# Optimization experiments

Measured on AMD Instinct MI355X. Metric: run time of the kernel, lower is better.

Reference implementation:

```python
import jax, jax.numpy as jnp
import numpy as np

N = 100000
E = 1600000
D = 128      # input_dim == hidden_dim
C = 40       # output_dim
L = 3        # num_layers
EPS = 1e-12  # F.normalize eps


def setup_inputs() -> dict:
    key = jax.random.key(0)
    ks = jax.random.split(key, 8)
    x = jax.random.normal(ks[0], (N, D), dtype=jnp.float32)
    edge_index = jax.random.randint(ks[1], (2, E), 0, N, dtype=jnp.int64)
    s = 1.0 / np.sqrt(D)
    # SAGEConv: lin_l (neighbor path, with bias), lin_r (root path, no bias)
    Wl = jax.random.uniform(ks[2], (L, D, D), jnp.float32, -s, s)
    bl = jax.random.uniform(ks[3], (L, D), jnp.float32, -s, s)
    Wr = jax.random.uniform(ks[4], (L, D, D), jnp.float32, -s, s)
    Wlin = jax.random.uniform(ks[5], (C, D), jnp.float32, -s, s)
    blin = jax.random.uniform(ks[6], (C,), jnp.float32, -s, s)
    return {"x": x, "edge_index": edge_index, "Wl": Wl, "bl": bl,
            "Wr": Wr, "Wlin": Wlin, "blin": blin}


def reference(x, edge_index, Wl, bl, Wr, Wlin, blin):
    src, dst = edge_index[0], edge_index[1]
    # in-degree counts for mean aggregation (computed once, reused per layer)
    cnt = jax.ops.segment_sum(jnp.ones((E,), jnp.float32), dst, num_segments=N)
    inv_cnt = (1.0 / jnp.maximum(cnt, 1.0))[:, None]  # [N,1]
    z = x
    for i in range(L):
        msg = z[src]  # gather [E, D]
        agg = jax.ops.segment_sum(msg, dst, num_segments=N) * inv_cnt  # mean [N, D]
        out = agg @ Wl[i].T + bl[i] + z @ Wr[i].T
        # SAGEConv normalize=True: L2 normalize per node
        nrm = jnp.linalg.norm(out, axis=-1, keepdims=True)
        out = out / jnp.maximum(nrm, EPS)
        z = jax.nn.relu(out)  # dropout p=0 -> identity
    return z @ Wlin.T + blin  # [N, C]
```

## Files before the change

### kernel.cpp

```cpp
#include <hip/hip_runtime.h>


typedef __bf16 bf16x8 __attribute__((ext_vector_type(8)));
typedef float  f32x4  __attribute__((ext_vector_type(4)));

#define MFMA16(a, b, c) __builtin_amdgcn_mfma_f32_16x16x32_bf16((a), (b), (c), 0, 0, 0)

__device__ __forceinline__ unsigned rne_bf16(float f) {
  unsigned u = __float_as_uint(f);
  unsigned r = u + 0x7FFFu + ((u >> 16) & 1u);
  return r >> 16;
}

__device__ __forceinline__ float bf_lo(unsigned u) { return __uint_as_float(u << 16); }
__device__ __forceinline__ float bf_hi(unsigned u) { return __uint_as_float(u & 0xFFFF0000u); }


__global__ __launch_bounds__(256) void histA_k(const int* __restrict__ dst,
                                               int* __restrict__ ghist, int E) {
  __shared__ int h[128];
  const int tid = threadIdx.x;
  if (tid < 128) h[tid] = 0;
  __syncthreads();
  const int e0 = blockIdx.x * 2048;
#pragma unroll
  for (int j = 0; j < 8; ++j) {
    int e = e0 + j * 256 + tid;
    if (e < E) atomicAdd(&h[dst[e] >> 10], 1);
  }
  __syncthreads();
  if (tid < 128 && h[tid]) atomicAdd(&ghist[tid], h[tid]);
}

__global__ void cscan_k(const int* __restrict__ ghist, int* __restrict__ cbase,
                        int* __restrict__ gcur, int E) {
  __shared__ int sd[128];
  const int tid = threadIdx.x;
  int v = ghist[tid];
  sd[tid] = v;
  __syncthreads();
  for (int off = 1; off < 128; off <<= 1) {
    int u = (tid >= off) ? sd[tid - off] : 0;
    __syncthreads();
    sd[tid] += u;
    __syncthreads();
  }
  int excl = sd[tid] - v;
  cbase[tid] = excl;
  gcur[tid] = excl;
  if (tid == 127) cbase[128] = sd[127];
}

__global__ __launch_bounds__(256) void bucketA_k(
    const int* __restrict__ src, const int* __restrict__ dst,
    int* __restrict__ gcur, unsigned* __restrict__ coarse, int E, int nc) {
  __shared__ int hist[128];
  __shared__ int sd[128];
  __shared__ int lpos[128];
  __shared__ int gbase[128];
  __shared__ unsigned stage[2048];
  __shared__ unsigned char sbuck[2048];

  const int tid = threadIdx.x;
  const int e0 = blockIdx.x * 2048;

  if (tid < 128) hist[tid] = 0;
  __syncthreads();

  int bv[8], pk[8];
#pragma unroll
  for (int j = 0; j < 8; ++j) {
    int e = e0 + j * 256 + tid;
    bv[j] = -1;
    if (e < E) {
      int s = src[e], d = dst[e];
      bv[j] = d >> 10;
      pk[j] = s | ((d & 1023) << 17);
      atomicAdd(&hist[bv[j]], 1);
    }
  }
  __syncthreads();

  if (tid < 128) sd[tid] = hist[tid];
  __syncthreads();
  for (int off = 1; off < 128; off <<= 1) {
    int t = 0;
    if (tid < 128 && tid >= off) t = sd[tid - off];
    __syncthreads();
    if (tid < 128) sd[tid] += t;
    __syncthreads();
  }
  if (tid < 128) {
    int excl = sd[tid] - hist[tid];
    lpos[tid] = excl;
    gbase[tid] = (tid < nc && hist[tid] > 0) ? atomicAdd(&gcur[tid], hist[tid]) : 0;
  }
  __syncthreads();

#pragma unroll
  for (int j = 0; j < 8; ++j) {
    if (bv[j] >= 0) {
      int slot = atomicAdd(&lpos[bv[j]], 1);
      stage[slot] = (unsigned)pk[j];
      sbuck[slot] = (unsigned char)bv[j];
    }
  }
  __syncthreads();

  const int total = sd[127];
  for (int i = tid; i < total; i += 256) {
    int b = sbuck[i];
    int excl = sd[b] - hist[b];
    coarse[gbase[b] + (i - excl)] = stage[i];
  }
}

__global__ __launch_bounds__(256) void bucketB_k(
    const int* __restrict__ cbase, const unsigned* __restrict__ coarse,
    int* __restrict__ esrc, int* __restrict__ offsets,
    float* __restrict__ inv_cnt, int n, int E) {
  __shared__ int hcnt[1024];
  __shared__ int cur[1024];
  __shared__ int sd[256];

  const int tid = threadIdx.x;
  const int b = blockIdx.x;
  const int base = b * 1024;
  const int nn = (n - base < 1024) ? (n - base) : 1024;
  const int cbeg = cbase[b];
  const int cend = cbase[b + 1];

  for (int j = tid; j < 1024; j += 256) hcnt[j] = 0;
  __syncthreads();
  for (int idx = cbeg + tid; idx < cend; idx += 256)
    atomicAdd(&hcnt[coarse[idx] >> 17], 1);
  __syncthreads();

  int b0 = hcnt[tid * 4], b1 = hcnt[tid * 4 + 1];
  int b2 = hcnt[tid * 4 + 2], b3 = hcnt[tid * 4 + 3];
  int tot = b0 + b1 + b2 + b3;
  sd[tid] = tot;
  __syncthreads();
  for (int off = 1; off < 256; off <<= 1) {
    int u = (tid >= off) ? sd[tid - off] : 0;
    __syncthreads();
    sd[tid] += u;
    __syncthreads();
  }
  int excl = cbeg + sd[tid] - tot;
  cur[tid * 4]     = excl;
  cur[tid * 4 + 1] = excl + b0;
  cur[tid * 4 + 2] = excl + b0 + b1;
  cur[tid * 4 + 3] = excl + b0 + b1 + b2;
  __syncthreads();

  for (int j = tid; j < nn; j += 256) {
    offsets[base + j] = cur[j];
    int c = hcnt[j] > 1 ? hcnt[j] : 1;
    inv_cnt[base + j] = 1.0f / (float)c;
  }
  if (tid == 0 && base + nn >= n) offsets[n] = cend;
  __syncthreads();

  for (int idx = cbeg + tid; idx < cend; idx += 256) {
    unsigned p = coarse[idx];
    int pos = atomicAdd(&cur[p >> 17], 1);
    esrc[pos] = (int)(p & 0x1FFFFu);
  }
}

__global__ void to_bf16_k(const float4* __restrict__ in, uint2* __restrict__ out, int n4) {
  int i = blockIdx.x * 256 + threadIdx.x;
  if (i >= n4) return;
  float4 f = in[i];
  uint2 o;
  o.x = rne_bf16(f.x) | (rne_bf16(f.y) << 16);
  o.y = rne_bf16(f.z) | (rne_bf16(f.w) << 16);
  out[i] = o;
}

__global__ void wfrag_prep_k(const float* __restrict__ Wl, const float* __restrict__ Wr,
                             unsigned short* __restrict__ wfrag) {
  int id = blockIdx.x * 256 + threadIdx.x;
  if (id >= 3 * 2 * 8 * 8 * 64) return;
  int l = id & 63;
  int c = (id >> 6) & 7;
  int t = (id >> 9) & 7;
  int p = (id >> 12) & 1;
  int layer = id >> 13;
  int col = t * 16 + (l & 15);
  int kbase = c * 32 + (l >> 4) * 8;
  unsigned short* dst = wfrag + (size_t)layer * 65536 +
                        ((((size_t)p * 8 + t) * 8 + c) * 64 + l) * 8;
#pragma unroll
  for (int j = 0; j < 8; ++j) {
    int k = kbase + j;
    float w = (k < 128) ? Wl[layer * 16384 + col * 128 + k]
                        : Wr[layer * 16384 + col * 128 + (k - 128)];
    unsigned h = rne_bf16(w);
    unsigned o;
    if (p == 0) o = h;
    else o = rne_bf16(w - __uint_as_float(h << 16));
    dst[j] = (unsigned short)o;
  }
}

__global__ void wlin_frag_k(const float* __restrict__ Wlin, unsigned short* __restrict__ wlf) {
  int id = blockIdx.x * 256 + threadIdx.x;
  if (id >= 3 * 4 * 64) return;
  int l = id & 63;
  int c = (id >> 6) & 3;
  int t = id >> 8;
  int col = t * 16 + (l & 15);
  int kbase = c * 32 + (l >> 4) * 8;
  unsigned short* dst = wlf + (size_t)id * 8;
#pragma unroll
  for (int j = 0; j < 8; ++j) {
    float w = (col < 40) ? Wlin[col * 128 + kbase + j] : 0.f;
    dst[j] = (unsigned short)rne_bf16(w);
  }
}

__global__ void aggregate_k(const unsigned short* __restrict__ zb,
                            const int* __restrict__ offsets,
                            const int* __restrict__ esrc,
                            const float* __restrict__ inv_cnt,
                            float* __restrict__ agg, int n) {
  int w = (blockIdx.x * 256 + threadIdx.x) >> 6;
  int lane = threadIdx.x & 63;
  if (w >= n) return;
  int beg = offsets[w], end = offsets[w + 1];
  int cnt = end - beg;
  int q = lane >> 4;
  int l16 = lane & 15;
  float a0 = 0.f, a1 = 0.f, a2 = 0.f, a3 = 0.f;
  float a4 = 0.f, a5 = 0.f, a6 = 0.f, a7 = 0.f;
  int t = 0;
  for (; t + 16 <= cnt; t += 16) {
#pragma unroll
    for (int u = 0; u < 4; ++u) {
      int s = esrc[beg + t + 4 * u + q];
      uint4 d = *(const uint4*)(zb + (size_t)s * 128 + l16 * 8);
      a0 += bf_lo(d.x); a1 += bf_hi(d.x);
      a2 += bf_lo(d.y); a3 += bf_hi(d.y);
      a4 += bf_lo(d.z); a5 += bf_hi(d.z);
      a6 += bf_lo(d.w); a7 += bf_hi(d.w);
    }
  }
  for (; t + 4 <= cnt; t += 4) {
    int s = esrc[beg + t + q];
    uint4 d = *(const uint4*)(zb + (size_t)s * 128 + l16 * 8);
    a0 += bf_lo(d.x); a1 += bf_hi(d.x);
    a2 += bf_lo(d.y); a3 += bf_hi(d.y);
    a4 += bf_lo(d.z); a5 += bf_hi(d.z);
    a6 += bf_lo(d.w); a7 += bf_hi(d.w);
  }
  if (t < cnt) {
    int e = t + q;
    float m = (e < cnt) ? 1.f : 0.f;
    int ec = (e < cnt) ? (beg + e) : (end - 1);
    int s = esrc[ec];
    uint4 d = *(const uint4*)(zb + (size_t)s * 128 + l16 * 8);
    a0 = fmaf(m, bf_lo(d.x), a0); a1 = fmaf(m, bf_hi(d.x), a1);
    a2 = fmaf(m, bf_lo(d.y), a2); a3 = fmaf(m, bf_hi(d.y), a3);
    a4 = fmaf(m, bf_lo(d.z), a4); a5 = fmaf(m, bf_hi(d.z), a5);
    a6 = fmaf(m, bf_lo(d.w), a6); a7 = fmaf(m, bf_hi(d.w), a7);
  }
#pragma unroll
  for (int m = 16; m <= 32; m <<= 1) {
    a0 += __shfl_xor(a0, m); a1 += __shfl_xor(a1, m);
    a2 += __shfl_xor(a2, m); a3 += __shfl_xor(a3, m);
    a4 += __shfl_xor(a4, m); a5 += __shfl_xor(a5, m);
    a6 += __shfl_xor(a6, m); a7 += __shfl_xor(a7, m);
  }
  if (q == 0) {
    float ic = inv_cnt[w];
    float* op = agg + (size_t)w * 128 + l16 * 8;
    *(float4*)op = make_float4(a0 * ic, a1 * ic, a2 * ic, a3 * ic);
    *(float4*)(op + 4) = make_float4(a4 * ic, a5 * ic, a6 * ic, a7 * ic);
  }
}

__global__ __launch_bounds__(256, 2) void sage_layer_mfma_k(
    const unsigned short* __restrict__ zb, const float* __restrict__ agg,
    const unsigned short* __restrict__ wf, const float* __restrict__ bl,
    unsigned short* __restrict__ out_bf, int n, int ntiles) {
  __shared__ unsigned short Ah_s[32 * 256];
  __shared__ unsigned short Al_s[32 * 128];
  __shared__ float psum[2][4][16];

  const int lane = threadIdx.x & 63;
  const int wv = threadIdx.x >> 6;
  const int g = lane >> 4;
  const int rl = lane & 15;

  const bf16x8* wfv = (const bf16x8*)wf;
  const int t0 = wv * 2, t1 = wv * 2 + 1;
  bf16x8 Bh0[8], Bh1[8], Bl0[8], Bl1[8];
#pragma unroll
  for (int c = 0; c < 8; ++c) {
    Bh0[c] = wfv[((0 * 8 + t0) * 8 + c) * 64 + lane];
    Bh1[c] = wfv[((0 * 8 + t1) * 8 + c) * 64 + lane];
    Bl0[c] = wfv[((1 * 8 + t0) * 8 + c) * 64 + lane];
    Bl1[c] = wfv[((1 * 8 + t1) * 8 + c) * 64 + lane];
  }
  const float b0 = bl[t0 * 16 + rl];
  const float b1 = bl[t1 * 16 + rl];

  char* pAh = (char*)Ah_s;
  char* pAl = (char*)Al_s;

  for (int tile = blockIdx.x; tile < ntiles; tile += gridDim.x) {
    const int v0 = tile * 32;

#pragma unroll
    for (int q = 0; q < 4; ++q) {
      int lin = q * 1024 + threadIdx.x * 4;
      int r = lin >> 7;
      int col = lin & 127;
      int v = v0 + r; v = (v < n) ? v : (n - 1);
      float4 f = *(const float4*)(agg + (size_t)v * 128 + col);
      unsigned h0 = rne_bf16(f.x), h1 = rne_bf16(f.y);
      unsigned h2 = rne_bf16(f.z), h3 = rne_bf16(f.w);
      unsigned l0 = rne_bf16(f.x - __uint_as_float(h0 << 16));
      unsigned l1 = rne_bf16(f.y - __uint_as_float(h1 << 16));
      unsigned l2 = rne_bf16(f.z - __uint_as_float(h2 << 16));
      unsigned l3 = rne_bf16(f.w - __uint_as_float(h3 << 16));
      int swz = (r & 7) << 4;
      int byteH = (r * 512 + col * 2) ^ swz;
      int byteL = (r * 256 + col * 2) ^ swz;
      *(uint2*)(pAh + byteH) = make_uint2(h0 | (h1 << 16), h2 | (h3 << 16));
      *(uint2*)(pAl + byteL) = make_uint2(l0 | (l1 << 16), l2 | (l3 << 16));
    }
#pragma unroll
    for (int q = 0; q < 2; ++q) {
      int lin = q * 2048 + threadIdx.x * 8;
      int r = lin >> 7;
      int col = lin & 127;
      int v = v0 + r; v = (v < n) ? v : (n - 1);
      uint4 d = *(const uint4*)(zb + (size_t)v * 128 + col);
      int byte = (r * 512 + 256 + col * 2) ^ ((r & 7) << 4);
      *(uint4*)(pAh + byte) = d;
    }
    __syncthreads();

#pragma unroll
    for (int s = 0; s < 2; ++s) {
      f32x4 a0 = {0.f, 0.f, 0.f, 0.f};
      f32x4 a1 = {0.f, 0.f, 0.f, 0.f};
      const int rowH = (s * 16 + rl) * 512;
      const int rowL = (s * 16 + rl) * 256;
      const int swz = (rl & 7) << 4;
#pragma unroll
      for (int c = 0; c < 4; ++c) {
        int offH = (rowH + c * 64 + g * 16) ^ swz;
        int offL = (rowL + c * 64 + g * 16) ^ swz;
        bf16x8 ah = *(const bf16x8*)(pAh + offH);
        bf16x8 al = *(const bf16x8*)(pAl + offL);
        a0 = MFMA16(ah, Bh0[c], a0); a1 = MFMA16(ah, Bh1[c], a1);
        a0 = MFMA16(ah, Bl0[c], a0); a1 = MFMA16(ah, Bl1[c], a1);
        a0 = MFMA16(al, Bh0[c], a0); a1 = MFMA16(al, Bh1[c], a1);
      }
#pragma unroll
      for (int c = 4; c < 8; ++c) {
        int offH = (rowH + c * 64 + g * 16) ^ swz;
        bf16x8 ah = *(const bf16x8*)(pAh + offH);
        a0 = MFMA16(ah, Bh0[c], a0); a1 = MFMA16(ah, Bh1[c], a1);
        a0 = MFMA16(ah, Bl0[c], a0); a1 = MFMA16(ah, Bl1[c], a1);
      }
      float pr[4];
#pragma unroll
      for (int j = 0; j < 4; ++j) {
        a0[j] += b0; a1[j] += b1;
        pr[j] = a0[j] * a0[j] + a1[j] * a1[j];
      }
#pragma unroll
      for (int m = 1; m < 16; m <<= 1) {
#pragma unroll
        for (int j = 0; j < 4; ++j) pr[j] += __shfl_xor(pr[j], m);
      }
      if (rl == 0) {
#pragma unroll
        for (int j = 0; j < 4; ++j) psum[s][wv][g * 4 + j] = pr[j];
      }
      __syncthreads();
#pragma unroll
      for (int j = 0; j < 4; ++j) {
        int row16 = g * 4 + j;
        float tot = psum[s][0][row16] + psum[s][1][row16] +
                    psum[s][2][row16] + psum[s][3][row16];
        float inv = 1.0f / fmaxf(sqrtf(tot), 1e-12f);
        int v = v0 + s * 16 + row16;
        if (v < n) {
          float o0 = fmaxf(a0[j] * inv, 0.f);
          float o1 = fmaxf(a1[j] * inv, 0.f);
          out_bf[(size_t)v * 128 + t0 * 16 + rl] = (unsigned short)rne_bf16(o0);
          out_bf[(size_t)v * 128 + t1 * 16 + rl] = (unsigned short)rne_bf16(o1);
        }
      }
    }
    __syncthreads();
  }
}

__global__ __launch_bounds__(256, 4) void final_linear_mfma_k(
    const unsigned short* __restrict__ zb, const unsigned short* __restrict__ wlf,
    const float* __restrict__ blin, float* __restrict__ out, int n, int ntiles) {
  __shared__ unsigned short Az[64 * 128];

  const int lane = threadIdx.x & 63;
  const int wv = threadIdx.x >> 6;
  const int g = lane >> 4;
  const int rl = lane & 15;

  const bf16x8* wv8 = (const bf16x8*)wlf;
  bf16x8 B[3][4];
#pragma unroll
  for (int t = 0; t < 3; ++t)
#pragma unroll
    for (int c = 0; c < 4; ++c) B[t][c] = wv8[(t * 4 + c) * 64 + lane];
  float bias[3];
#pragma unroll
  for (int t = 0; t < 3; ++t) {
    int col = t * 16 + rl;
    bias[t] = (col < 40) ? blin[col] : 0.f;
  }

  char* pAz = (char*)Az;

  for (int tile = blockIdx.x; tile < ntiles; tile += gridDim.x) {
    const int v0 = tile * 64;
#pragma unroll
    for (int q = 0; q < 4; ++q) {
      int lin = q * 2048 + threadIdx.x * 8;
      int r = lin >> 7;
      int col = lin & 127;
      int v = v0 + r; v = (v < n) ? v : (n - 1);
      uint4 d = *(const uint4*)(zb + (size_t)v * 128 + col);
      int byte = (r * 256 + col * 2) ^ ((r & 7) << 4);
      *(uint4*)(pAz + byte) = d;
    }
    __syncthreads();

    f32x4 acc0 = {0.f, 0.f, 0.f, 0.f};
    f32x4 acc1 = {0.f, 0.f, 0.f, 0.f};
    f32x4 acc2 = {0.f, 0.f, 0.f, 0.f};
    const int rowB = (wv * 16 + rl) * 256;
    const int swz = (rl & 7) << 4;
#pragma unroll
    for (int c = 0; c < 4; ++c) {
      int off = (rowB + c * 64 + g * 16) ^ swz;
      bf16x8 a = *(const bf16x8*)(pAz + off);
      acc0 = MFMA16(a, B[0][c], acc0);
      acc1 = MFMA16(a, B[1][c], acc1);
      acc2 = MFMA16(a, B[2][c], acc2);
    }
#pragma unroll
    for (int j = 0; j < 4; ++j) {
      int v = v0 + wv * 16 + g * 4 + j;
      if (v < n) {
        float* op = out + (size_t)v * 40;
        op[rl] = acc0[j] + bias[0];
        op[16 + rl] = acc1[j] + bias[1];
        if (rl < 8) op[32 + rl] = acc2[j] + bias[2];
      }
    }
    __syncthreads();
  }
}


extern "C" void kernel_launch(void* const* d_in, const int* in_sizes, int n_in,
                              void* d_out, int out_size, void* d_ws, size_t ws_size,
                              hipStream_t stream) {
  const float* x    = (const float*)d_in[0];
  const int*   ei   = (const int*)d_in[1];
  const float* Wl   = (const float*)d_in[2];
  const float* bl   = (const float*)d_in[3];
  const float* Wr   = (const float*)d_in[4];
  const float* Wlin = (const float*)d_in[5];
  const float* blin = (const float*)d_in[6];

  const int N = in_sizes[0] / 128;
  const int E = in_sizes[1] / 2;
  const int D = 128;
  const int NC = (N + 1023) >> 10;

  const int* src = ei;
  const int* dstp = ei + E;

  unsigned short* planeA = (unsigned short*)d_ws;
  unsigned short* planeB = planeA + (size_t)N * D;
  float* bufA    = (float*)(planeB + (size_t)N * D);
  float* inv_cnt = bufA + (size_t)N * D;
  unsigned short* wlf = (unsigned short*)(inv_cnt + N);
  unsigned short* Wfrag = wlf + 6144;
  int*   offsets = (int*)(Wfrag + 3 * 65536);
  int*   esrc    = offsets + N + 1;
  unsigned* coarse = (unsigned*)(esrc + E);
  int*   cbase   = (int*)(coarse + E);
  int*   gcur    = cbase + 129;
  int*   ghist   = gcur + 128;

  hipMemsetAsync(ghist, 0, 128 * 4, stream);
  histA_k<<<(E + 2047) / 2048, 256, 0, stream>>>(dstp, ghist, E);
  cscan_k<<<1, 128, 0, stream>>>(ghist, cbase, gcur, E);
  bucketA_k<<<(E + 2047) / 2048, 256, 0, stream>>>(src, dstp, gcur, coarse, E, NC);
  bucketB_k<<<NC, 256, 0, stream>>>(cbase, coarse, esrc, offsets, inv_cnt, N, E);

  wfrag_prep_k<<<96, 256, 0, stream>>>(Wl, Wr, Wfrag);
  wlin_frag_k<<<3, 256, 0, stream>>>(Wlin, wlf);
  to_bf16_k<<<((N * 32) + 255) / 256, 256, 0, stream>>>((const float4*)x, (uint2*)planeA, N * 32);

  const int aggGrid = (int)(((size_t)N * 64 + 255) / 256);
  const int ntiles = (N + 31) / 32;
  const int sageGrid = 512;

  aggregate_k<<<aggGrid, 256, 0, stream>>>(planeA, offsets, esrc, inv_cnt, bufA, N);
  sage_layer_mfma_k<<<sageGrid, 256, 0, stream>>>(planeA, bufA, Wfrag + 0 * 65536, bl + 0 * D, planeB, N, ntiles);
  aggregate_k<<<aggGrid, 256, 0, stream>>>(planeB, offsets, esrc, inv_cnt, bufA, N);
  sage_layer_mfma_k<<<sageGrid, 256, 0, stream>>>(planeB, bufA, Wfrag + 1 * 65536, bl + 1 * D, planeA, N, ntiles);
  aggregate_k<<<aggGrid, 256, 0, stream>>>(planeA, offsets, esrc, inv_cnt, bufA, N);
  sage_layer_mfma_k<<<sageGrid, 256, 0, stream>>>(planeA, bufA, Wfrag + 2 * 65536, bl + 2 * D, planeB, N, ntiles);

  const int ntiles64 = (N + 63) / 64;
  final_linear_mfma_k<<<ntiles64, 256, 0, stream>>>(planeB, wlf, blin, (float*)d_out, N, ntiles64);
}
```

Measured before the change: 416.1 us.

## Aggregate with 16 lanes per node and emit pre-split bf16 hi/lo pairs

The aggregation kernel now gives each node a 16-lane group instead of a full 64-lane wavefront. Each group walks its edges serially, two at a time, so the cross-quarter shuffle reduction and the idle lanes on low-degree nodes go away. The aggregate is written as packed hi/lo bf16 pairs, which moves the split-precision conversion out of the MFMA layer kernel. The layer kernel is also retuned to launch_bounds occupancy 4 with a grid of 1024. The trade-off is less memory-level parallelism per node, since each group has at most two outstanding gathers. High-degree nodes now take longer serial chains.

```diff
diff --git a/kernel.cpp b/kernel.cpp
--- a/kernel.cpp
+++ b/kernel.cpp
@@ -14,6 +14,12 @@
 
 __device__ __forceinline__ float bf_lo(unsigned u) { return __uint_as_float(u << 16); }
 __device__ __forceinline__ float bf_hi(unsigned u) { return __uint_as_float(u & 0xFFFF0000u); }
+
+__device__ __forceinline__ unsigned pack_hl(float f) {
+  unsigned h = rne_bf16(f);
+  unsigned l = rne_bf16(f - __uint_as_float(h << 16));
+  return (h << 16) | l;
+}
 
 
 __global__ __launch_bounds__(256) void histA_k(const int* __restrict__ dst,
@@ -225,64 +231,48 @@
                             const int* __restrict__ offsets,
                             const int* __restrict__ esrc,
                             const float* __restrict__ inv_cnt,
-                            float* __restrict__ agg, int n) {
-  int w = (blockIdx.x * 256 + threadIdx.x) >> 6;
-  int lane = threadIdx.x & 63;
-  if (w >= n) return;
-  int beg = offsets[w], end = offsets[w + 1];
-  int cnt = end - beg;
-  int q = lane >> 4;
-  int l16 = lane & 15;
+                            unsigned* __restrict__ aggp, int n) {
+  int node = (blockIdx.x * 256 + threadIdx.x) >> 4;
+  int l16 = threadIdx.x & 15;
+  if (node >= n) return;
+  int beg = offsets[node], end = offsets[node + 1];
   float a0 = 0.f, a1 = 0.f, a2 = 0.f, a3 = 0.f;
   float a4 = 0.f, a5 = 0.f, a6 = 0.f, a7 = 0.f;
-  int t = 0;
-  for (; t + 16 <= cnt; t += 16) {
-#pragma unroll
-    for (int u = 0; u < 4; ++u) {
-      int s = esrc[beg + t + 4 * u + q];
-      uint4 d = *(const uint4*)(zb + (size_t)s * 128 + l16 * 8);
-      a0 += bf_lo(d.x); a1 += bf_hi(d.x);
-      a2 += bf_lo(d.y); a3 += bf_hi(d.y);
-      a4 += bf_lo(d.z); a5 += bf_hi(d.z);
-      a6 += bf_lo(d.w); a7 += bf_hi(d.w);
-    }
-  }
-  for (; t + 4 <= cnt; t += 4) {
-    int s = esrc[beg + t + q];
-    uint4 d = *(const uint4*)(zb + (size_t)s * 128 + l16 * 8);
-    a0 += bf_lo(d.x); a1 += bf_hi(d.x);
-    a2 += bf_lo(d.y); a3 += bf_hi(d.y);
-    a4 += bf_lo(d.z); a5 += bf_hi(d.z);
-    a6 += bf_lo(d.w); a7 += bf_hi(d.w);
-  }
-  if (t < cnt) {
-    int e = t + q;
-    float m = (e < cnt) ? 1.f : 0.f;
-    int ec = (e < cnt) ? (beg + e) : (end - 1);
-    int s = esrc[ec];
-    uint4 d = *(const uint4*)(zb + (size_t)s * 128 + l16 * 8);
-    a0 = fmaf(m, bf_lo(d.x), a0); a1 = fmaf(m, bf_hi(d.x), a1);
-    a2 = fmaf(m, bf_lo(d.y), a2); a3 = fmaf(m, bf_hi(d.y), a3);
-    a4 = fmaf(m, bf_lo(d.z), a4); a5 = fmaf(m, bf_hi(d.z), a5);
-    a6 = fmaf(m, bf_lo(d.w), a6); a7 = fmaf(m, bf_hi(d.w), a7);
-  }
-#pragma unroll
-  for (int m = 16; m <= 32; m <<= 1) {
-    a0 += __shfl_xor(a0, m); a1 += __shfl_xor(a1, m);
-    a2 += __shfl_xor(a2, m); a3 += __shfl_xor(a3, m);
-    a4 += __shfl_xor(a4, m); a5 += __shfl_xor(a5, m);
-    a6 += __shfl_xor(a6, m); a7 += __shfl_xor(a7, m);
-  }
-  if (q == 0) {
-    float ic = inv_cnt[w];
-    float* op = agg + (size_t)w * 128 + l16 * 8;
-    *(float4*)op = make_float4(a0 * ic, a1 * ic, a2 * ic, a3 * ic);
-    *(float4*)(op + 4) = make_float4(a4 * ic, a5 * ic, a6 * ic, a7 * ic);
-  }
-}
-
-__global__ __launch_bounds__(256, 2) void sage_layer_mfma_k(
-    const unsigned short* __restrict__ zb, const float* __restrict__ agg,
+  int t = beg;
+  for (; t + 2 <= end; t += 2) {
+    int s0 = esrc[t], s1 = esrc[t + 1];
+    uint4 d0 = *(const uint4*)(zb + (size_t)s0 * 128 + l16 * 8);
+    uint4 d1 = *(const uint4*)(zb + (size_t)s1 * 128 + l16 * 8);
+    a0 += bf_lo(d0.x); a1 += bf_hi(d0.x);
+    a2 += bf_lo(d0.y); a3 += bf_hi(d0.y);
+    a4 += bf_lo(d0.z); a5 += bf_hi(d0.z);
+    a6 += bf_lo(d0.w); a7 += bf_hi(d0.w);
+    a0 += bf_lo(d1.x); a1 += bf_hi(d1.x);
+    a2 += bf_lo(d1.y); a3 += bf_hi(d1.y);
+    a4 += bf_lo(d1.z); a5 += bf_hi(d1.z);
+    a6 += bf_lo(d1.w); a7 += bf_hi(d1.w);
+  }
+  if (t < end) {
+    int s0 = esrc[t];
+    uint4 d0 = *(const uint4*)(zb + (size_t)s0 * 128 + l16 * 8);
+    a0 += bf_lo(d0.x); a1 += bf_hi(d0.x);
+    a2 += bf_lo(d0.y); a3 += bf_hi(d0.y);
+    a4 += bf_lo(d0.z); a5 += bf_hi(d0.z);
+    a6 += bf_lo(d0.w); a7 += bf_hi(d0.w);
+  }
+  float ic = inv_cnt[node];
+  unsigned* op = aggp + (size_t)node * 128 + l16 * 8;
+  uint4 o0, o1;
+  o0.x = pack_hl(a0 * ic); o0.y = pack_hl(a1 * ic);
+  o0.z = pack_hl(a2 * ic); o0.w = pack_hl(a3 * ic);
+  o1.x = pack_hl(a4 * ic); o1.y = pack_hl(a5 * ic);
+  o1.z = pack_hl(a6 * ic); o1.w = pack_hl(a7 * ic);
+  *(uint4*)op = o0;
+  *(uint4*)(op + 4) = o1;
+}
+
+__global__ __launch_bounds__(256, 4) void sage_layer_mfma_k(
+    const unsigned short* __restrict__ zb, const unsigned* __restrict__ aggp,
     const unsigned short* __restrict__ wf, const float* __restrict__ bl,
     unsigned short* __restrict__ out_bf, int n, int ntiles) {
   __shared__ unsigned short Ah_s[32 * 256];
@@ -319,18 +309,15 @@
       int r = lin >> 7;
       int col = lin & 127;
       int v = v0 + r; v = (v < n) ? v : (n - 1);
-      float4 f = *(const float4*)(agg + (size_t)v * 128 + col);
-      unsigned h0 = rne_bf16(f.x), h1 = rne_bf16(f.y);
-      unsigned h2 = rne_bf16(f.z), h3 = rne_bf16(f.w);
-      unsigned l0 = rne_bf16(f.x - __uint_as_float(h0 << 16));
-      unsigned l1 = rne_bf16(f.y - __uint_as_float(h1 << 16));
-      unsigned l2 = rne_bf16(f.z - __uint_as_float(h2 << 16));
-      unsigned l3 = rne_bf16(f.w - __uint_as_float(h3 << 16));
+      uint4 p = *(const uint4*)(aggp + (size_t)v * 128 + col);
+      uint2 hw, lw;
+      hw.x = (p.x >> 16) | (p.y & 0xFFFF0000u);
+      hw.y = (p.z >> 16) | (p.w & 0xFFFF0000u);
+      lw.x = (p.x & 0xFFFFu) | (p.y << 16);
+      lw.y = (p.z & 0xFFFFu) | (p.w << 16);
       int swz = (r & 7) << 4;
-      int byteH = (r * 512 + col * 2) ^ swz;
-      int byteL = (r * 256 + col * 2) ^ swz;
-      *(uint2*)(pAh + byteH) = make_uint2(h0 | (h1 << 16), h2 | (h3 << 16));
-      *(uint2*)(pAl + byteL) = make_uint2(l0 | (l1 << 16), l2 | (l3 << 16));
+      *(uint2*)(pAh + ((r * 512 + col * 2) ^ swz)) = hw;
+      *(uint2*)(pAl + ((r * 256 + col * 2) ^ swz)) = lw;
     }
 #pragma unroll
     for (int q = 0; q < 2; ++q) {
@@ -491,8 +478,8 @@
 
   unsigned short* planeA = (unsigned short*)d_ws;
   unsigned short* planeB = planeA + (size_t)N * D;
-  float* bufA    = (float*)(planeB + (size_t)N * D);
-  float* inv_cnt = bufA + (size_t)N * D;
+  unsigned* aggp = (unsigned*)(planeB + (size_t)N * D);
+  float* inv_cnt = (float*)(aggp + (size_t)N * D);
   unsigned short* wlf = (unsigned short*)(inv_cnt + N);
   unsigned short* Wfrag = wlf + 6144;
   int*   offsets = (int*)(Wfrag + 3 * 65536);
@@ -512,16 +499,16 @@
   wlin_frag_k<<<3, 256, 0, stream>>>(Wlin, wlf);
   to_bf16_k<<<((N * 32) + 255) / 256, 256, 0, stream>>>((const float4*)x, (uint2*)planeA, N * 32);
 
-  const int aggGrid = (int)(((size_t)N * 64 + 255) / 256);
+  const int aggGrid = (N * 16 + 255) / 256;
   const int ntiles = (N + 31) / 32;
-  const int sageGrid = 512;
-
-  aggregate_k<<<aggGrid, 256, 0, stream>>>(planeA, offsets, esrc, inv_cnt, bufA, N);
-  sage_layer_mfma_k<<<sageGrid, 256, 0, stream>>>(planeA, bufA, Wfrag + 0 * 65536, bl + 0 * D, planeB, N, ntiles);
-  aggregate_k<<<aggGrid, 256, 0, stream>>>(planeB, offsets, esrc, inv_cnt, bufA, N);
-  sage_layer_mfma_k<<<sageGrid, 256, 0, stream>>>(planeB, bufA, Wfrag + 1 * 65536, bl + 1 * D, planeA, N, ntiles);
-  aggregate_k<<<aggGrid, 256, 0, stream>>>(planeA, offsets, esrc, inv_cnt, bufA, N);
-  sage_layer_mfma_k<<<sageGrid, 256, 0, stream>>>(planeA, bufA, Wfrag + 2 * 65536, bl + 2 * D, planeB, N, ntiles);
+  const int sageGrid = 1024;
+
+  aggregate_k<<<aggGrid, 256, 0, stream>>>(planeA, offsets, esrc, inv_cnt, aggp, N);
+  sage_layer_mfma_k<<<sageGrid, 256, 0, stream>>>(planeA, aggp, Wfrag + 0 * 65536, bl + 0 * D, planeB, N, ntiles);
+  aggregate_k<<<aggGrid, 256, 0, stream>>>(planeB, offsets, esrc, inv_cnt, aggp, N);
+  sage_layer_mfma_k<<<sageGrid, 256, 0, stream>>>(planeB, aggp, Wfrag + 1 * 65536, bl + 1 * D, planeA, N, ntiles);
+  aggregate_k<<<aggGrid, 256, 0, stream>>>(planeA, offsets, esrc, inv_cnt, aggp, N);
+  sage_layer_mfma_k<<<sageGrid, 256, 0, stream>>>(planeA, aggp, Wfrag + 2 * 65536, bl + 2 * D, planeB, N, ntiles);
 
   const int ntiles64 = (N + 63) / 64;
   final_linear_mfma_k<<<ntiles64, 256, 0, stream>>>(planeB, wlf, blin, (float*)d_out, N, ntiles64);
```

Result: slower. 628.4 us (+51.0%).
